# Performance work log

Hardware: AMD Instinct MI355X
Metric: run time of the kernel (lower is better)

The kernel has to match this reference:

```python
import jax, jax.numpy as jnp
import numpy as np

DIM = 256
K = 4096
TAU_HI = 2.0
TAU_LO = 0.5
TAU_DECAY_STEPS = 10000.0
EPS_NORM = 1e-12


def _l2_normalize(x):
    n = jnp.linalg.norm(x, axis=-1, keepdims=True)
    return x / jnp.maximum(n, EPS_NORM)


def setup_inputs() -> dict:
    key = jax.random.key(0)
    k1, k2, k3, k4 = jax.random.split(key, 4)
    B, T = 16, 1024
    z = jax.random.normal(k1, (B, T, DIM), dtype=jnp.float32)
    u = jax.random.uniform(k2, (B, T, K), dtype=jnp.float32)          # gumbel base noise
    codebook = jax.random.normal(k3, (K, DIM), dtype=jnp.float32)
    codebook_usage = jax.random.uniform(k4, (K,), dtype=jnp.float32)
    return {"z": z, "u": u, "codebook": codebook,
            "codebook_usage": codebook_usage, "step": 100}


def reference(z, u, codebook, codebook_usage, step):
    B, T, D = z.shape
    # temperature schedule: tau = tau_lo + (tau_hi - tau_lo) * exp(-step/decay)
    tau = TAU_LO + (TAU_HI - TAU_LO) * jnp.exp(-jnp.float32(step) / TAU_DECAY_STEPS)

    # cosine distance: 1 - <z_hat, c_hat>
    z_flat = z.reshape(-1, D)                      # [N, D]
    z_n = _l2_normalize(z_flat)
    c_n = _l2_normalize(codebook)                  # [K, D]
    cosine_sim = jnp.einsum('nd,kd->nk', z_n, c_n) # [N, K]
    distances = (1.0 - cosine_sim).reshape(B, T, K)

    # gumbel-softmax with straight-through one-hot
    logits = -distances
    gumbel = -jnp.log(-jnp.log(u + 1e-10) + 1e-10)
    soft_codes = jax.nn.softmax((logits + gumbel) / tau, axis=-1)   # [B, T, K]
    indices = jnp.argmax(soft_codes, axis=-1)                       # [B, T]
    hard_codes = jax.nn.one_hot(indices, K, dtype=soft_codes.dtype)
    codes = hard_codes - jax.lax.stop_gradient(soft_codes) + soft_codes

    quantized = jnp.einsum('btk,kd->btd', codes, codebook)          # [B, T, D]
    embedding = codebook[indices]                                    # gather [B, T, D]

    # straight-through to encoder input
    z_q = z + jax.lax.stop_gradient(quantized - z)
    commitment = 0.5 * jnp.mean((jax.lax.stop_gradient(z_q) - z) ** 2)

    # usage entropy / perplexity from usage buffer
    usage_sum = jnp.sum(codebook_usage)
    usage_prob = jnp.where(usage_sum > 0,
                           codebook_usage / (usage_sum + 1e-10),
                           jnp.full_like(codebook_usage, 1.0 / K))
    entropy = -jnp.sum(usage_prob * jnp.log(usage_prob + 1e-10))
    perplexity = jnp.exp(entropy)

    # entropy bonus uses step AFTER the in-place increment in torch
    step_after = step + 1
    bonus_weight = 0.05 * (1.0 - step_after / 20000.0)
    entropy_bonus = jnp.where(step_after < 20000,
                              -bonus_weight * entropy,
                              jnp.float32(0.0))

    return (z_q, embedding, indices, commitment, entropy_bonus, perplexity, entropy)
```

## Files before the change

### kernel.cpp

```cpp
#include <hip/hip_runtime.h>
#include <cstdint>
#include <cstddef>

#define N_ROWS 16384
#define KCODES 4096
#define DIM    256
#define CAP    128

__global__ __launch_bounds__(256) void cinv_kernel(
    const float* __restrict__ cb, float* __restrict__ cinv)
{
    int r    = blockIdx.x * 4 + (threadIdx.x >> 6);
    int lane = threadIdx.x & 63;
    float4 v = reinterpret_cast<const float4*>(cb + (size_t)r * DIM)[lane];
    float s = v.x*v.x + v.y*v.y + v.z*v.z + v.w*v.w;
    #pragma unroll
    for (int m = 1; m <= 32; m <<= 1) s += __shfl_xor(s, m);
    if (lane == 0) cinv[r] = 1.0f / fmaxf(sqrtf(s), 1e-12f);
}

__global__ __launch_bounds__(256) void row_kernel(
    const float* __restrict__ u, const float* __restrict__ z,
    const float* __restrict__ cb, const float* __restrict__ cinv,
    float* __restrict__ zq, float* __restrict__ emb,
    float* __restrict__ idx_out, float* __restrict__ commit_part)
{
    const int row  = blockIdx.x;
    const int t    = threadIdx.x, lane = t & 63, wave = t >> 6;

    __shared__ float2 cand[CAP];
    __shared__ int    s_cnt;
    __shared__ float  s_max[4];
    __shared__ float  s_bestv[4];
    __shared__ int    s_besti[4];

    if (t == 0) s_cnt = 0;

    const float4* ur4 = reinterpret_cast<const float4*>(u + (size_t)row * KCODES);
    float4 v[4];
    #pragma unroll
    for (int k = 0; k < 4; ++k) v[k] = ur4[k * 256 + t];

    float um = -1.0f;
    #pragma unroll
    for (int k = 0; k < 4; ++k)
        um = fmaxf(um, fmaxf(fmaxf(v[k].x, v[k].y), fmaxf(v[k].z, v[k].w)));
    #pragma unroll
    for (int m = 1; m <= 32; m <<= 1) um = fmaxf(um, __shfl_xor(um, m));
    if (lane == 0) s_max[wave] = um;
    __syncthreads();
    const float umax = fmaxf(fmaxf(s_max[0], s_max[1]), fmaxf(s_max[2], s_max[3]));

    const float gmax  = -logf(-logf(umax + 1e-10f) + 1e-10f);
    const float y_thr = expf(-(gmax - 2.06f)) - 1e-10f;
    float u_thr = expf(-y_thr) - 1e-10f;
    u_thr = u_thr - fabsf(u_thr) * 2e-6f - 1e-12f;

    #pragma unroll
    for (int k = 0; k < 4; ++k) {
        float vv[4] = {v[k].x, v[k].y, v[k].z, v[k].w};
        #pragma unroll
        for (int e = 0; e < 4; ++e) {
            if (vv[e] >= u_thr) {
                int pos = atomicAdd(&s_cnt, 1);
                if (pos < CAP)
                    cand[pos] = make_float2(vv[e], (float)((k * 256 + t) * 4 + e));
            }
        }
    }
    __syncthreads();
    const int n = s_cnt;

    float4 zv = reinterpret_cast<const float4*>(z + (size_t)row * DIM)[lane];
    float ss = zv.x*zv.x + zv.y*zv.y + zv.z*zv.z + zv.w*zv.w;
    #pragma unroll
    for (int m = 1; m <= 32; m <<= 1) ss += __shfl_xor(ss, m);
    const float zinv = 1.0f / fmaxf(sqrtf(ss), 1e-12f);
    float4 zn;
    zn.x = zv.x*zinv; zn.y = zv.y*zinv; zn.z = zv.z*zinv; zn.w = zv.w*zinv;

    float best = -3.0e38f;
    int   bi   = 1 << 30;

    auto evalc = [&](float uu, int col) {
        float4 cv = reinterpret_cast<const float4*>(cb + (size_t)col * DIM)[lane];
        float civ = cinv[col];
        float d = zn.x*(cv.x*civ) + zn.y*(cv.y*civ) + zn.z*(cv.z*civ) + zn.w*(cv.w*civ);
        #pragma unroll
        for (int m = 1; m <= 32; m <<= 1) d += __shfl_xor(d, m);
        float y1 = -logf(uu + 1e-10f);
        float g  = -logf(y1 + 1e-10f);
        float val = (d - 1.0f) + g;
        if (val > best || (val == best && col < bi)) { best = val; bi = col; }
    };

    if (n <= CAP) {
        for (int c = wave; c < n; c += 4) {
            float2 cd = cand[c];
            evalc(cd.x, (int)cd.y);
        }
    } else {
        const float* urow = u + (size_t)row * KCODES;
        for (int col = wave; col < KCODES; col += 4) evalc(urow[col], col);
    }
    if (lane == 0) { s_bestv[wave] = best; s_besti[wave] = bi; }
    __syncthreads();

    best = s_bestv[0]; bi = s_besti[0];
    #pragma unroll
    for (int w = 1; w < 4; ++w) {
        float ov = s_bestv[w]; int oi = s_besti[w];
        if (ov > best || (ov == best && oi < bi)) { best = ov; bi = oi; }
    }
    if (wave == 0) {
        float4 cw = reinterpret_cast<const float4*>(cb + (size_t)bi * DIM)[lane];
        reinterpret_cast<float4*>(zq + (size_t)row * DIM)[lane] = cw;
        float dx = cw.x - zv.x, dy = cw.y - zv.y, dz = cw.z - zv.z, dw = cw.w - zv.w;
        float s2 = dx*dx + dy*dy + dz*dz + dw*dw;
        #pragma unroll
        for (int m = 1; m <= 32; m <<= 1) s2 += __shfl_xor(s2, m);
        if (lane == 0) {
            idx_out[row]     = (float)bi;
            commit_part[row] = s2;
        }
    } else if (wave == 1) {
        float4 cw = reinterpret_cast<const float4*>(cb + (size_t)bi * DIM)[lane];
        reinterpret_cast<float4*>(emb + (size_t)row * DIM)[lane] = cw;
    }
}

__global__ __launch_bounds__(256) void commit_reduce_kernel(
    const float* __restrict__ commit_part, float* __restrict__ commit_acc)
{
    __shared__ float red[256];
    const int t = threadIdx.x;
    float4 v = reinterpret_cast<const float4*>(commit_part)[blockIdx.x * 256 + t];
    red[t] = v.x + v.y + v.z + v.w;
    __syncthreads();
    for (int w = 128; w > 0; w >>= 1) { if (t < w) red[t] += red[t + w]; __syncthreads(); }
    if (t == 0) atomicAdd(commit_acc, red[0]);
}

__global__ __launch_bounds__(256) void scalars_kernel(
    const float* __restrict__ commit_acc, const float* __restrict__ usage,
    const int* __restrict__ step_ptr, float* __restrict__ out4)
{
    __shared__ float red[256];
    int t = threadIdx.x;

    float us = 0.f;
    for (int i = t; i < KCODES; i += 256) us += usage[i];
    red[t] = us; __syncthreads();
    for (int w = 128; w > 0; w >>= 1) { if (t < w) red[t] += red[t + w]; __syncthreads(); }
    float usage_sum = red[0];
    __syncthreads();

    float e = 0.f;
    for (int i = t; i < KCODES; i += 256) {
        float p = (usage_sum > 0.f) ? usage[i] / (usage_sum + 1e-10f) : (1.0f / KCODES);
        e += p * logf(p + 1e-10f);
    }
    red[t] = e; __syncthreads();
    for (int w = 128; w > 0; w >>= 1) { if (t < w) red[t] += red[t + w]; __syncthreads(); }

    if (t == 0) {
        float entropy = -red[0];
        int step_after = step_ptr[0] + 1;
        float bonus_w = 0.05f * (1.0f - (float)step_after / 20000.0f);
        float eb = (step_after < 20000) ? (-bonus_w * entropy) : 0.0f;
        out4[0] = 0.5f * commit_acc[0] / 4194304.0f;
        out4[1] = eb;
        out4[2] = expf(entropy);
        out4[3] = entropy;
    }
}

extern "C" void kernel_launch(void* const* d_in, const int* in_sizes, int n_in,
                              void* d_out, int out_size, void* d_ws, size_t ws_size,
                              hipStream_t stream)
{
    const float* z     = (const float*)d_in[0];
    const float* u     = (const float*)d_in[1];
    const float* cb    = (const float*)d_in[2];
    const float* usage = (const float*)d_in[3];
    const int*   step  = (const int*)d_in[4];

    float* out  = (float*)d_out;
    float* zq   = out;
    float* emb  = out + 4194304;
    float* idxo = out + 8388608;
    float* scal = out + 8404992;

    float* ws          = (float*)d_ws;
    float* cinv        = ws;
    float* commit_part = ws + 4096;
    float* commit_acc  = ws + 20480;

    hipMemsetAsync(commit_acc, 0, sizeof(float), stream);
    hipLaunchKernelGGL(cinv_kernel, dim3(1024), dim3(256), 0, stream, cb, cinv);
    hipLaunchKernelGGL(row_kernel, dim3(N_ROWS), dim3(256), 0, stream,
                       u, z, cb, cinv, zq, emb, idxo, commit_part);
    hipLaunchKernelGGL(commit_reduce_kernel, dim3(16), dim3(256), 0, stream,
                       commit_part, commit_acc);
    hipLaunchKernelGGL(scalars_kernel, dim3(1), dim3(256), 0, stream,
                       commit_acc, usage, step, scal);
}
```

Measured before the change: 95.36 us.

## Process one row per wave with per-lane top-4 candidate filtering

Each wave now handles a whole row instead of one row per 256-thread block. Each lane keeps a running top-4 of its u values, and candidate evaluation uses ballot/shuffle within the wave. This removes the shared-memory atomics, the candidate buffer and the block-level syncs. If the 4th-best of any lane passes the threshold, the wave rescans the row from global memory. The single-wave design serialises the dot-product evaluations and adds per-element compare and select work during the scan.

```diff
diff --git a/kernel.cpp b/kernel.cpp
--- a/kernel.cpp
+++ b/kernel.cpp
@@ -5,7 +5,6 @@
 #define N_ROWS 16384
 #define KCODES 4096
 #define DIM    256
-#define CAP    128
 
 __global__ __launch_bounds__(256) void cinv_kernel(
     const float* __restrict__ cb, float* __restrict__ cinv)
@@ -25,51 +24,40 @@
     float* __restrict__ zq, float* __restrict__ emb,
     float* __restrict__ idx_out, float* __restrict__ commit_part)
 {
-    const int row  = blockIdx.x;
-    const int t    = threadIdx.x, lane = t & 63, wave = t >> 6;
-
-    __shared__ float2 cand[CAP];
-    __shared__ int    s_cnt;
-    __shared__ float  s_max[4];
-    __shared__ float  s_bestv[4];
-    __shared__ int    s_besti[4];
-
-    if (t == 0) s_cnt = 0;
+    const int row  = blockIdx.x * 4 + (threadIdx.x >> 6);
+    const int lane = threadIdx.x & 63;
 
     const float4* ur4 = reinterpret_cast<const float4*>(u + (size_t)row * KCODES);
-    float4 v[4];
-    #pragma unroll
-    for (int k = 0; k < 4; ++k) v[k] = ur4[k * 256 + t];
-
-    float um = -1.0f;
-    #pragma unroll
-    for (int k = 0; k < 4; ++k)
-        um = fmaxf(um, fmaxf(fmaxf(v[k].x, v[k].y), fmaxf(v[k].z, v[k].w)));
-    #pragma unroll
-    for (int m = 1; m <= 32; m <<= 1) um = fmaxf(um, __shfl_xor(um, m));
-    if (lane == 0) s_max[wave] = um;
-    __syncthreads();
-    const float umax = fmaxf(fmaxf(s_max[0], s_max[1]), fmaxf(s_max[2], s_max[3]));
-
-    const float gmax  = -logf(-logf(umax + 1e-10f) + 1e-10f);
-    const float y_thr = expf(-(gmax - 2.06f)) - 1e-10f;
-    float u_thr = expf(-y_thr) - 1e-10f;
-    u_thr = u_thr - fabsf(u_thr) * 2e-6f - 1e-12f;
-
-    #pragma unroll
-    for (int k = 0; k < 4; ++k) {
-        float vv[4] = {v[k].x, v[k].y, v[k].z, v[k].w};
-        #pragma unroll
-        for (int e = 0; e < 4; ++e) {
-            if (vv[e] >= u_thr) {
-                int pos = atomicAdd(&s_cnt, 1);
-                if (pos < CAP)
-                    cand[pos] = make_float2(vv[e], (float)((k * 256 + t) * 4 + e));
+
+    float tv0 = -1.f, tv1 = -1.f, tv2 = -1.f, tv3 = -1.f;
+    int   tc0 = 0,    tc1 = 0,    tc2 = 0,    tc3 = 0;
+
+    #pragma unroll 2
+    for (int cc = 0; cc < 4; ++cc) {
+        float4 v[4];
+        #pragma unroll
+        for (int j = 0; j < 4; ++j) v[j] = ur4[(cc * 4 + j) * 64 + lane];
+        #pragma unroll
+        for (int j = 0; j < 4; ++j) {
+            const int base = ((cc * 4 + j) * 64 + lane) * 4;
+            float xs[4] = {v[j].x, v[j].y, v[j].z, v[j].w};
+            #pragma unroll
+            for (int e = 0; e < 4; ++e) {
+                float x = xs[e];
+                float mn = fminf(fminf(tv0, tv1), fminf(tv2, tv3));
+                if (x > mn) {
+                    if      (tv0 == mn) { tv0 = x; tc0 = base + e; }
+                    else if (tv1 == mn) { tv1 = x; tc1 = base + e; }
+                    else if (tv2 == mn) { tv2 = x; tc2 = base + e; }
+                    else                { tv3 = x; tc3 = base + e; }
+                }
             }
         }
     }
-    __syncthreads();
-    const int n = s_cnt;
+
+    float um = fmaxf(fmaxf(tv0, tv1), fmaxf(tv2, tv3));
+    #pragma unroll
+    for (int m = 1; m <= 32; m <<= 1) um = fmaxf(um, __shfl_xor(um, m));
 
     float4 zv = reinterpret_cast<const float4*>(z + (size_t)row * DIM)[lane];
     float ss = zv.x*zv.x + zv.y*zv.y + zv.z*zv.z + zv.w*zv.w;
@@ -78,6 +66,11 @@
     const float zinv = 1.0f / fmaxf(sqrtf(ss), 1e-12f);
     float4 zn;
     zn.x = zv.x*zinv; zn.y = zv.y*zinv; zn.z = zv.z*zinv; zn.w = zv.w*zinv;
+
+    const float gmax  = -logf(-logf(um + 1e-10f) + 1e-10f);
+    const float y_thr = expf(-(gmax - 2.06f)) - 1e-10f;
+    float u_thr = expf(-y_thr) - 1e-10f;
+    u_thr = u_thr - fabsf(u_thr) * 2e-6f - 1e-12f;
 
     float best = -3.0e38f;
     int   bi   = 1 << 30;
@@ -94,38 +87,49 @@
         if (val > best || (val == best && col < bi)) { best = val; bi = col; }
     };
 
-    if (n <= CAP) {
-        for (int c = wave; c < n; c += 4) {
-            float2 cd = cand[c];
-            evalc(cd.x, (int)cd.y);
+    const float m4 = fminf(fminf(tv0, tv1), fminf(tv2, tv3));
+    if (__ballot(m4 >= u_thr)) {
+        for (int c = 0; c < 16; ++c) {
+            float4 vv = ur4[c * 64 + lane];
+            float xs[4] = {vv.x, vv.y, vv.z, vv.w};
+            #pragma unroll
+            for (int e = 0; e < 4; ++e) {
+                unsigned long long mm = __ballot(xs[e] >= u_thr);
+                while (mm) {
+                    int src = __ffsll(mm) - 1;
+                    mm &= mm - 1;
+                    float uu = __shfl(xs[e], src);
+                    int  col = (c * 64 + src) * 4 + e;
+                    evalc(uu, col);
+                }
+            }
         }
     } else {
-        const float* urow = u + (size_t)row * KCODES;
-        for (int col = wave; col < KCODES; col += 4) evalc(urow[col], col);
-    }
-    if (lane == 0) { s_bestv[wave] = best; s_besti[wave] = bi; }
-    __syncthreads();
-
-    best = s_bestv[0]; bi = s_besti[0];
-    #pragma unroll
-    for (int w = 1; w < 4; ++w) {
-        float ov = s_bestv[w]; int oi = s_besti[w];
-        if (ov > best || (ov == best && oi < bi)) { best = ov; bi = oi; }
-    }
-    if (wave == 0) {
-        float4 cw = reinterpret_cast<const float4*>(cb + (size_t)bi * DIM)[lane];
-        reinterpret_cast<float4*>(zq + (size_t)row * DIM)[lane] = cw;
-        float dx = cw.x - zv.x, dy = cw.y - zv.y, dz = cw.z - zv.z, dw = cw.w - zv.w;
-        float s2 = dx*dx + dy*dy + dz*dz + dw*dw;
-        #pragma unroll
-        for (int m = 1; m <= 32; m <<= 1) s2 += __shfl_xor(s2, m);
-        if (lane == 0) {
-            idx_out[row]     = (float)bi;
-            commit_part[row] = s2;
+        float tvs[4] = {tv0, tv1, tv2, tv3};
+        int   tcs[4] = {tc0, tc1, tc2, tc3};
+        #pragma unroll
+        for (int j = 0; j < 4; ++j) {
+            unsigned long long mm = __ballot(tvs[j] >= u_thr);
+            while (mm) {
+                int src = __ffsll(mm) - 1;
+                mm &= mm - 1;
+                float uu = __shfl(tvs[j], src);
+                int  col = __shfl(tcs[j], src);
+                evalc(uu, col);
+            }
         }
-    } else if (wave == 1) {
-        float4 cw = reinterpret_cast<const float4*>(cb + (size_t)bi * DIM)[lane];
-        reinterpret_cast<float4*>(emb + (size_t)row * DIM)[lane] = cw;
+    }
+
+    float4 cw = reinterpret_cast<const float4*>(cb + (size_t)bi * DIM)[lane];
+    reinterpret_cast<float4*>(zq  + (size_t)row * DIM)[lane] = cw;
+    reinterpret_cast<float4*>(emb + (size_t)row * DIM)[lane] = cw;
+    float dx = cw.x - zv.x, dy = cw.y - zv.y, dz = cw.z - zv.z, dw = cw.w - zv.w;
+    float s2 = dx*dx + dy*dy + dz*dz + dw*dw;
+    #pragma unroll
+    for (int m = 1; m <= 32; m <<= 1) s2 += __shfl_xor(s2, m);
+    if (lane == 0) {
+        idx_out[row]     = (float)bi;
+        commit_part[row] = s2;
     }
 }
 
@@ -198,7 +202,7 @@
 
     hipMemsetAsync(commit_acc, 0, sizeof(float), stream);
     hipLaunchKernelGGL(cinv_kernel, dim3(1024), dim3(256), 0, stream, cb, cinv);
-    hipLaunchKernelGGL(row_kernel, dim3(N_ROWS), dim3(256), 0, stream,
+    hipLaunchKernelGGL(row_kernel, dim3(N_ROWS / 4), dim3(256), 0, stream,
                        u, z, cb, cinv, zq, emb, idxo, commit_part);
     hipLaunchKernelGGL(commit_reduce_kernel, dim3(16), dim3(256), 0, stream,
                        commit_part, commit_acc);
```

New measurement: 117.1 us. 1.23x slower.

## Split row kernel into separate scan and select kernels via global candidate buffer

Applied to the files above, without the earlier changes.

The fused per-row kernel is split in two. A scan kernel streams u, computes the threshold and appends candidates to a global per-row buffer using global atomics. A select kernel then reads the candidates back and evaluates their cosine distances against the codebook. The overflow fallback now recomputes the threshold and skips columns below it. The intent seems to be to separate the bandwidth-bound scan from the latency-bound gather phase. In exchange it adds an extra launch, a memset, global atomics, and a global round trip for the candidate data.

```diff
diff --git a/kernel.cpp b/kernel.cpp
--- a/kernel.cpp
+++ b/kernel.cpp
@@ -19,22 +19,14 @@
     if (lane == 0) cinv[r] = 1.0f / fmaxf(sqrtf(s), 1e-12f);
 }
 
-__global__ __launch_bounds__(256) void row_kernel(
-    const float* __restrict__ u, const float* __restrict__ z,
-    const float* __restrict__ cb, const float* __restrict__ cinv,
-    float* __restrict__ zq, float* __restrict__ emb,
-    float* __restrict__ idx_out, float* __restrict__ commit_part)
+__global__ __launch_bounds__(256) void scan_kernel(
+    const float* __restrict__ u, int* __restrict__ gcnt,
+    float2* __restrict__ gcand)
 {
     const int row  = blockIdx.x;
     const int t    = threadIdx.x, lane = t & 63, wave = t >> 6;
 
-    __shared__ float2 cand[CAP];
-    __shared__ int    s_cnt;
-    __shared__ float  s_max[4];
-    __shared__ float  s_bestv[4];
-    __shared__ int    s_besti[4];
-
-    if (t == 0) s_cnt = 0;
+    __shared__ float s_max[4];
 
     const float4* ur4 = reinterpret_cast<const float4*>(u + (size_t)row * KCODES);
     float4 v[4];
@@ -62,14 +54,29 @@
         #pragma unroll
         for (int e = 0; e < 4; ++e) {
             if (vv[e] >= u_thr) {
-                int pos = atomicAdd(&s_cnt, 1);
+                int pos = atomicAdd(&gcnt[row], 1);
                 if (pos < CAP)
-                    cand[pos] = make_float2(vv[e], (float)((k * 256 + t) * 4 + e));
+                    gcand[(size_t)row * CAP + pos] =
+                        make_float2(vv[e], (float)((k * 256 + t) * 4 + e));
             }
         }
     }
-    __syncthreads();
-    const int n = s_cnt;
+}
+
+__global__ __launch_bounds__(256) void select_kernel(
+    const float* __restrict__ u, const float* __restrict__ z,
+    const float* __restrict__ cb, const float* __restrict__ cinv,
+    const int* __restrict__ gcnt, const float2* __restrict__ gcand,
+    float* __restrict__ zq, float* __restrict__ emb,
+    float* __restrict__ idx_out, float* __restrict__ commit_part)
+{
+    const int row  = blockIdx.x;
+    const int t    = threadIdx.x, lane = t & 63, wave = t >> 6;
+
+    __shared__ float s_bestv[4];
+    __shared__ int   s_besti[4];
+
+    const int n = gcnt[row];
 
     float4 zv = reinterpret_cast<const float4*>(z + (size_t)row * DIM)[lane];
     float ss = zv.x*zv.x + zv.y*zv.y + zv.z*zv.z + zv.w*zv.w;
@@ -96,12 +103,31 @@
 
     if (n <= CAP) {
         for (int c = wave; c < n; c += 4) {
-            float2 cd = cand[c];
+            float2 cd = gcand[(size_t)row * CAP + c];
             evalc(cd.x, (int)cd.y);
         }
     } else {
+        const float4* ur4 = reinterpret_cast<const float4*>(u + (size_t)row * KCODES);
+        float um = -1.0f;
+        for (int k = 0; k < 4; ++k) {
+            float4 vv = ur4[k * 256 + t];
+            um = fmaxf(um, fmaxf(fmaxf(vv.x, vv.y), fmaxf(vv.z, vv.w)));
+        }
+        #pragma unroll
+        for (int m = 1; m <= 32; m <<= 1) um = fmaxf(um, __shfl_xor(um, m));
+        __shared__ float s_fmax[4];
+        if (lane == 0) s_fmax[wave] = um;
+        __syncthreads();
+        const float umax = fmaxf(fmaxf(s_fmax[0], s_fmax[1]), fmaxf(s_fmax[2], s_fmax[3]));
+        const float gmax  = -logf(-logf(umax + 1e-10f) + 1e-10f);
+        const float y_thr = expf(-(gmax - 2.06f)) - 1e-10f;
+        float u_thr = expf(-y_thr) - 1e-10f;
+        u_thr = u_thr - fabsf(u_thr) * 2e-6f - 1e-12f;
         const float* urow = u + (size_t)row * KCODES;
-        for (int col = wave; col < KCODES; col += 4) evalc(urow[col], col);
+        for (int col = wave; col < KCODES; col += 4) {
+            float uu = urow[col];
+            if (uu >= u_thr) evalc(uu, col);
+        }
     }
     if (lane == 0) { s_bestv[wave] = best; s_besti[wave] = bi; }
     __syncthreads();
@@ -191,15 +217,20 @@
     float* idxo = out + 8388608;
     float* scal = out + 8404992;
 
-    float* ws          = (float*)d_ws;
-    float* cinv        = ws;
-    float* commit_part = ws + 4096;
-    float* commit_acc  = ws + 20480;
+    float*  ws          = (float*)d_ws;
+    float*  cinv        = ws;
+    float*  commit_part = ws + 4096;
+    float*  commit_acc  = ws + 20480;
+    int*    gcnt        = (int*)(ws + 20608);
+    float2* gcand       = (float2*)(ws + 36992);
 
     hipMemsetAsync(commit_acc, 0, sizeof(float), stream);
+    hipMemsetAsync(gcnt, 0, N_ROWS * sizeof(int), stream);
     hipLaunchKernelGGL(cinv_kernel, dim3(1024), dim3(256), 0, stream, cb, cinv);
-    hipLaunchKernelGGL(row_kernel, dim3(N_ROWS), dim3(256), 0, stream,
-                       u, z, cb, cinv, zq, emb, idxo, commit_part);
+    hipLaunchKernelGGL(scan_kernel, dim3(N_ROWS), dim3(256), 0, stream,
+                       u, gcnt, gcand);
+    hipLaunchKernelGGL(select_kernel, dim3(N_ROWS), dim3(256), 0, stream,
+                       u, z, cb, cinv, gcnt, gcand, zq, emb, idxo, commit_part);
     hipLaunchKernelGGL(commit_reduce_kernel, dim3(16), dim3(256), 0, stream,
                        commit_part, commit_acc);
     hipLaunchKernelGGL(scalars_kernel, dim3(1), dim3(256), 0, stream,
```

After: 121.9 us. 27.8% more time.
